# Kernel tuning notes

Hardware: AMD Instinct MI355X
Metric: run time of the kernel (lower is better)

The kernel has to match this reference:

```python
import jax, jax.numpy as jnp
import numpy as np


def setup_inputs() -> dict:
    key = jax.random.key(0)
    ks = jax.random.split(key, 8)
    C, dk = 256, 32
    B, H, W = 4, 64, 64
    x = jax.random.normal(ks[0], (B, C, H, W), dtype=jnp.float32)
    wq = jax.random.normal(ks[1], (dk, C), dtype=jnp.float32) * (1.0 / np.sqrt(C))
    bq = jnp.zeros((dk,), dtype=jnp.float32)
    wk = jax.random.normal(ks[2], (dk, C), dtype=jnp.float32) * (1.0 / np.sqrt(C))
    bk = jnp.zeros((dk,), dtype=jnp.float32)
    wv = jax.random.normal(ks[3], (C, C), dtype=jnp.float32) * (1.0 / np.sqrt(C))
    bv = jnp.zeros((C,), dtype=jnp.float32)
    gamma = jnp.ones((1,), dtype=jnp.float32)
    return {"x": x, "wq": wq, "bq": bq, "wk": wk, "bk": bk,
            "wv": wv, "bv": bv, "gamma": gamma}


def reference(x, wq, bq, wk, bk, wv, bv, gamma):
    B, C, H, W = x.shape
    N = H * W
    xf = x.reshape(B, C, N)  # [B, C, N]
    # 1x1 convs == per-pixel linear projections
    q = jnp.einsum('dc,bcn->bnd', wq, xf) + bq  # [B, N, dk]  (proj_query, permuted)
    k = jnp.einsum('dc,bcn->bdn', wk, xf) + bk[None, :, None]  # [B, dk, N]
    v = jnp.einsum('ec,bcn->ben', wv, xf) + bv[None, :, None]  # [B, C, N]
    energy = jnp.einsum('bnd,bdm->bnm', q, k)  # [B, N, N]
    attention = jax.nn.softmax(energy, axis=-1)
    # out[b,c,i] = sum_j v[b,c,j] * attention[b,i,j]
    out = jnp.einsum('bcj,bij->bci', v, attention)  # [B, C, N]
    out = out.reshape(B, C, H, W)
    return gamma[0] * out + x
```

## Files before the change

### kernel.cpp

```cpp
#include <hip/hip_runtime.h>

#define NPIX 4096
#define CIN  256
#define DK   32

typedef __attribute__((ext_vector_type(8))) short short8;
typedef __attribute__((ext_vector_type(16))) float f32x16;

__device__ __forceinline__ unsigned short f2bf(float f) {
    unsigned int u = __float_as_uint(f);
    return (unsigned short)((u + 0x7fffu + ((u >> 16) & 1u)) >> 16);
}
__device__ __forceinline__ float bf2f(unsigned short h) {
    return __uint_as_float(((unsigned int)h) << 16);
}

__global__ void wprep_kernel(const float* __restrict__ wq, const float* __restrict__ wk,
                             const float* __restrict__ wv,
                             unsigned short* __restrict__ wqh, unsigned short* __restrict__ wql,
                             unsigned short* __restrict__ wkh, unsigned short* __restrict__ wkl,
                             unsigned short* __restrict__ wvh) {
    const int lane = threadIdx.x & 63, li = lane & 31, hi = lane >> 5;
    const int kc = blockIdx.x, y = blockIdx.y;
    if (y < 4) {
        const float* m = (y < 2) ? wq : wk;
        short8 h8, l8;
#pragma unroll
        for (int e = 0; e < 8; ++e) {
            float v = m[li * CIN + kc * 16 + hi * 8 + e];
            unsigned short hb = f2bf(v);
            h8[e] = (short)hb;
            l8[e] = (short)f2bf(v - bf2f(hb));
        }
        unsigned short* dst = (y == 0) ? wqh : (y == 1) ? wql : (y == 2) ? wkh : wkl;
        *reinterpret_cast<short8*>(&dst[kc * 512 + lane * 8]) = (y & 1) ? l8 : h8;
    } else {
        const int cblk = y - 4;
        short8 h8;
#pragma unroll
        for (int e = 0; e < 8; ++e)
            h8[e] = (short)f2bf(wv[(cblk * 32 + li) * CIN + kc * 16 + hi * 8 + e]);
        *reinterpret_cast<short8*>(&wvh[(cblk * 16 + kc) * 512 + lane * 8]) = h8;
    }
}

__global__ __launch_bounds__(512) void projall_kernel(
        const float* __restrict__ x,
        const unsigned short* __restrict__ wqh, const unsigned short* __restrict__ wql,
        const unsigned short* __restrict__ wkh, const unsigned short* __restrict__ wkl,
        const unsigned short* __restrict__ wvh,
        const float* __restrict__ bq, const float* __restrict__ bk, const float* __restrict__ bv,
        unsigned short* __restrict__ qfrag, unsigned short* __restrict__ kfrag,
        unsigned short* __restrict__ vfrag) {
    __shared__ float xs[64][36];
    __shared__ unsigned short xhf[16 * 512];
    __shared__ unsigned short xlf[16 * 512];
    __shared__ unsigned short ts[2][32][40];

    const int t = threadIdx.x, lane = t & 63, li = lane & 31, hi = lane >> 5, w = t >> 6;
    const int nblk = blockIdx.x, b = blockIdx.y;
    const int n0 = nblk * 32;

    for (int cb = 0; cb < 4; ++cb) {
        {
            int c = t >> 3, n4 = (t & 7) * 4;
            float4 v = *reinterpret_cast<const float4*>(
                &x[(size_t)(b * CIN + cb * 64 + c) * NPIX + n0 + n4]);
            xs[c][n4 + 0] = v.x; xs[c][n4 + 1] = v.y;
            xs[c][n4 + 2] = v.z; xs[c][n4 + 3] = v.w;
        }
        __syncthreads();
        {
            const int kc = w & 3;
            const bool isL = (w >= 4);
            short8 f;
#pragma unroll
            for (int e = 0; e < 8; ++e) {
                float v = xs[kc * 16 + hi * 8 + e][li];
                unsigned short hb = f2bf(v);
                f[e] = isL ? (short)f2bf(v - bf2f(hb)) : (short)hb;
            }
            unsigned short* dst = isL ? xlf : xhf;
            *reinterpret_cast<short8*>(&dst[(cb * 4 + kc) * 512 + lane * 8]) = f;
        }
        __syncthreads();
    }

    if (w < 2) {
        const unsigned short* wh = (w == 0) ? wqh : wkh;
        const unsigned short* wl = (w == 0) ? wql : wkl;
        const float* bias = (w == 0) ? bq : bk;
        f32x16 acc;
#pragma unroll
        for (int r = 0; r < 16; ++r) acc[r] = 0.f;
        for (int kc = 0; kc < 16; ++kc) {
            short8 ah = *reinterpret_cast<const short8*>(&xhf[kc * 512 + lane * 8]);
            short8 al = *reinterpret_cast<const short8*>(&xlf[kc * 512 + lane * 8]);
            short8 whf = *reinterpret_cast<const short8*>(&wh[kc * 512 + lane * 8]);
            short8 wlf = *reinterpret_cast<const short8*>(&wl[kc * 512 + lane * 8]);
            acc = __builtin_amdgcn_mfma_f32_32x32x16_bf16(ah, whf, acc, 0, 0, 0);
            acc = __builtin_amdgcn_mfma_f32_32x32x16_bf16(al, whf, acc, 0, 0, 0);
            acc = __builtin_amdgcn_mfma_f32_32x32x16_bf16(ah, wlf, acc, 0, 0, 0);
        }
        const float bs = bias[li];
#pragma unroll
        for (int r = 0; r < 16; ++r) {
            int row = (r & 3) + 8 * (r >> 2) + 4 * hi;
            ts[w][row][li] = f2bf(acc[r] + bs);
        }
        unsigned short* dstf = (w == 0) ? qfrag : kfrag;
#pragma unroll
        for (int dh = 0; dh < 2; ++dh) {
            short8 f = *reinterpret_cast<const short8*>(&ts[w][li][dh * 16 + hi * 8]);
            *reinterpret_cast<short8*>(
                &dstf[((size_t)(b * 128 + nblk) * 2 + dh) * 512 + lane * 8]) = f;
        }
    } else {
        const int w2 = w - 2;
        const int njob = (w2 < 2) ? 2 : 1;
        for (int jj = 0; jj < njob; ++jj) {
            const int cblk = w2 + jj * 6;
            f32x16 acc;
#pragma unroll
            for (int r = 0; r < 16; ++r) acc[r] = 0.f;
            for (int kc = 0; kc < 16; ++kc) {
                short8 xb = *reinterpret_cast<const short8*>(&xhf[kc * 512 + lane * 8]);
                short8 wf = *reinterpret_cast<const short8*>(&wvh[(cblk * 16 + kc) * 512 + lane * 8]);
                acc = __builtin_amdgcn_mfma_f32_32x32x16_bf16(xb, wf, acc, 0, 0, 0);
            }
            const float bvv = bv[cblk * 32 + li];
#pragma unroll
            for (int g = 0; g < 2; ++g) {
                short8 sv;
#pragma unroll
                for (int e = 0; e < 8; ++e) sv[e] = (short)f2bf(acc[g * 8 + e] + bvv);
                *reinterpret_cast<short8*>(
                    &vfrag[((size_t)(b * 8 + cblk) * 256 + nblk * 2 + g) * 512 + lane * 8]) = sv;
            }
        }
    }
}

__global__ __launch_bounds__(768, 6) void attnv_kernel(
        const unsigned short* __restrict__ qfrag, const unsigned short* __restrict__ kfrag,
        const unsigned short* __restrict__ vfrag, unsigned short* __restrict__ opart,
        float* __restrict__ lpart, float* __restrict__ out) {
    __shared__ unsigned short Ps[4 * 8 * 512];
    __shared__ float sred[2][4][32];

    const int t = threadIdx.x, lane = t & 63, li = lane & 31, hi = lane >> 5, w = t >> 6;
    const int blk = blockIdx.x;
    const int xcd = blk & 7, slot = blk >> 3;
    const int jh = slot & 1, ps = slot >> 1;
    const int b = xcd >> 1;
    const int ipos = (xcd & 1) * 32 + ps;

    if (w < 4) {
        const int sl = w & 3;
        short8 qb[2][2];
#pragma unroll
        for (int it = 0; it < 2; ++it) {
            size_t qoff = ((size_t)(b * 128 + ipos * 2 + it) * 2) * 512 + lane * 8;
            qb[it][0] = *reinterpret_cast<const short8*>(&qfrag[qoff]);
            qb[it][1] = *reinterpret_cast<const short8*>(&qfrag[qoff + 512]);
        }
        float ssum[2] = {0.f, 0.f};

        auto do_E = [&](int s) {
            const int buf = s & 1;
            size_t koff = ((size_t)(b * 128 + jh * 64 + s * 4 + sl) * 2) * 512 + lane * 8;
            short8 k0 = *reinterpret_cast<const short8*>(&kfrag[koff]);
            short8 k1 = *reinterpret_cast<const short8*>(&kfrag[koff + 512]);
#pragma unroll
            for (int it = 0; it < 2; ++it) {
                f32x16 e;
#pragma unroll
                for (int r = 0; r < 16; ++r) e[r] = 0.f;
                e = __builtin_amdgcn_mfma_f32_32x32x16_bf16(k0, qb[it][0], e, 0, 0, 0);
                e = __builtin_amdgcn_mfma_f32_32x32x16_bf16(k1, qb[it][1], e, 0, 0, 0);
#pragma unroll
                for (int g = 0; g < 2; ++g) {
                    short8 pv8;
#pragma unroll
                    for (int e2 = 0; e2 < 8; ++e2) {
                        float pe = __expf(e[g * 8 + e2]);
                        ssum[it] += pe;
                        pv8[e2] = (short)f2bf(pe);
                    }
                    *reinterpret_cast<short8*>(
                        &Ps[((it * 2 + buf) * 8 + sl * 2 + g) * 512 + lane * 8]) = pv8;
                }
            }
        };

        do_E(0);
        __syncthreads();
#pragma unroll 1
        for (int s = 0; s < 16; ++s) {
            if (s + 1 < 16) do_E(s + 1);
            __syncthreads();
        }
#pragma unroll
        for (int it = 0; it < 2; ++it) {
            ssum[it] += __shfl_xor(ssum[it], 32);
            if (lane < 32) sred[it][sl][li] = ssum[it];
        }
        __syncthreads();
        if (sl == 0 && lane < 32) {
#pragma unroll
            for (int it = 0; it < 2; ++it) {
                float lt = sred[it][0][li] + sred[it][1][li] + sred[it][2][li] + sred[it][3][li];
                lpart[((size_t)jh * 4 + b) * NPIX + ipos * 64 + it * 32 + li] = lt;
            }
        }
    } else {
        const int cq = w - 4;
        f32x16 acc0, acc1;
#pragma unroll
        for (int r = 0; r < 16; ++r) { acc0[r] = 0.f; acc1[r] = 0.f; }

        __syncthreads();
#pragma unroll 1
        for (int s = 0; s < 16; ++s) {
            const int buf = s & 1;
            size_t vbase = ((size_t)(b * 8 + cq) * 256 + jh * 128 + s * 8) * 512 + lane * 8;
            short8 vcur = *reinterpret_cast<const short8*>(&vfrag[vbase]);
#pragma unroll
            for (int kc = 0; kc < 8; ++kc) {
                short8 vnext;
                if (kc < 7) vnext = *reinterpret_cast<const short8*>(&vfrag[vbase + (kc + 1) * 512]);
                short8 B0 = *reinterpret_cast<const short8*>(&Ps[(buf * 8 + kc) * 512 + lane * 8]);
                short8 B1 = *reinterpret_cast<const short8*>(&Ps[((2 + buf) * 8 + kc) * 512 + lane * 8]);
                acc0 = __builtin_amdgcn_mfma_f32_32x32x16_bf16(vcur, B0, acc0, 0, 0, 0);
                acc1 = __builtin_amdgcn_mfma_f32_32x32x16_bf16(vcur, B1, acc1, 0, 0, 0);
                vcur = vnext;
            }
            __syncthreads();
        }
        __syncthreads();

#pragma unroll
        for (int it = 0; it < 2; ++it) {
            const f32x16& A = it ? acc1 : acc0;
#pragma unroll
            for (int r = 0; r < 16; ++r) {
                int c = cq * 32 + (r & 3) + 8 * (r >> 2) + 4 * hi;
                size_t idx = (size_t)(b * CIN + c) * NPIX + ipos * 64 + it * 32 + li;
                if (jh == 0) out[idx] = A[r];
                else         opart[idx] = f2bf(A[r]);
            }
        }
    }
}

__global__ __launch_bounds__(256) void merge_kernel(
        const unsigned short* __restrict__ opart, const float* __restrict__ lpart,
        const float* __restrict__ xin, const float* __restrict__ gamma,
        float* __restrict__ out) {
    const size_t idx4 = ((size_t)blockIdx.x * 256 + threadIdx.x) * 4;
    const size_t i  = idx4 & (NPIX - 1);
    const size_t b  = idx4 >> 20;
    float4 o0 = *reinterpret_cast<const float4*>(&out[idx4]);
    float4 xv = *reinterpret_cast<const float4*>(&xin[idx4]);
    float4 l0 = *reinterpret_cast<const float4*>(&lpart[b * NPIX + i]);
    float4 l1 = *reinterpret_cast<const float4*>(&lpart[(4 + b) * NPIX + i]);
    const unsigned short* op = &opart[idx4];
    const float g = gamma[0];
    float4 o;
    o.x = g * (o0.x + bf2f(op[0])) / (l0.x + l1.x) + xv.x;
    o.y = g * (o0.y + bf2f(op[1])) / (l0.y + l1.y) + xv.y;
    o.z = g * (o0.z + bf2f(op[2])) / (l0.z + l1.z) + xv.z;
    o.w = g * (o0.w + bf2f(op[3])) / (l0.w + l1.w) + xv.w;
    *reinterpret_cast<float4*>(&out[idx4]) = o;
}

extern "C" void kernel_launch(void* const* d_in, const int* in_sizes, int n_in,
                              void* d_out, int out_size, void* d_ws, size_t ws_size,
                              hipStream_t stream) {
    const float* x     = (const float*)d_in[0];
    const float* wq    = (const float*)d_in[1];
    const float* bq    = (const float*)d_in[2];
    const float* wk    = (const float*)d_in[3];
    const float* bk    = (const float*)d_in[4];
    const float* wv    = (const float*)d_in[5];
    const float* bv    = (const float*)d_in[6];
    const float* gamma = (const float*)d_in[7];
    float* out = (float*)d_out;

    unsigned short* qf    = (unsigned short*)d_ws;
    unsigned short* kf    = qf + (size_t)524288;
    unsigned short* vf    = kf + (size_t)524288;
    unsigned short* wqh   = vf + (size_t)4194304;
    unsigned short* wql   = wqh + 8192;
    unsigned short* wkh   = wql + 8192;
    unsigned short* wkl   = wkh + 8192;
    unsigned short* wvh   = wkl + 8192;
    unsigned short* opart = wvh + 65536;
    float*          lpart = (float*)(opart + 4194304);

    wprep_kernel<<<dim3(16, 12), 64, 0, stream>>>(wq, wk, wv, wqh, wql, wkh, wkl, wvh);
    projall_kernel<<<dim3(128, 4), 512, 0, stream>>>(x, wqh, wql, wkh, wkl, wvh,
                                                     bq, bk, bv, qf, kf, vf);
    attnv_kernel<<<dim3(512), 768, 0, stream>>>(qf, kf, vf, opart, lpart, out);
    merge_kernel<<<dim3(4096), 256, 0, stream>>>(opart, lpart, x, gamma, out);
}
```

Before: 145.4 us.

## Give each PV wave two channel blocks and shrink attention block to 512 threads

The attention kernel drops from 8 consumer waves (one 32-channel block each) to 4 consumer waves that each own two channel blocks. Each P fragment read from LDS now feeds four MFMAs instead of two, halving LDS traffic per MFMA, and the block becomes 512 threads with adjusted launch bounds. The exp/bf16 packing also switches to a paired float2-to-bf16x2 intrinsic with a tree sum. The cost is more accumulator registers per wave, and the explicit software prefetch of V fragments is gone, so global load latency may be less hidden.

Measured after the change: 143.6 us. Within noise of the previous version (-1.2%).

```diff
diff --git a/kernel.cpp b/kernel.cpp
--- a/kernel.cpp
+++ b/kernel.cpp
@@ -1,4 +1,5 @@
 #include <hip/hip_runtime.h>
+#include <hip/hip_bf16.h>
 
 #define NPIX 4096
 #define CIN  256
@@ -13,6 +14,12 @@
 }
 __device__ __forceinline__ float bf2f(unsigned short h) {
     return __uint_as_float(((unsigned int)h) << 16);
+}
+__device__ __forceinline__ unsigned int f2bf2(float a, float b) {
+    __hip_bfloat162 h = __float22bfloat162_rn(make_float2(a, b));
+    unsigned int u;
+    __builtin_memcpy(&u, &h, 4);
+    return u;
 }
 
 __global__ void wprep_kernel(const float* __restrict__ wq, const float* __restrict__ wk,
@@ -141,7 +148,7 @@
     }
 }
 
-__global__ __launch_bounds__(768, 6) void attnv_kernel(
+__global__ __launch_bounds__(512, 4) void attnv_kernel(
         const unsigned short* __restrict__ qfrag, const unsigned short* __restrict__ kfrag,
         const unsigned short* __restrict__ vfrag, unsigned short* __restrict__ opart,
         float* __restrict__ lpart, float* __restrict__ out) {
@@ -156,7 +163,7 @@
     const int ipos = (xcd & 1) * 32 + ps;
 
     if (w < 4) {
-        const int sl = w & 3;
+        const int sl = w;
         short8 qb[2][2];
 #pragma unroll
         for (int it = 0; it < 2; ++it) {
@@ -180,15 +187,16 @@
                 e = __builtin_amdgcn_mfma_f32_32x32x16_bf16(k1, qb[it][1], e, 0, 0, 0);
 #pragma unroll
                 for (int g = 0; g < 2; ++g) {
-                    short8 pv8;
-#pragma unroll
-                    for (int e2 = 0; e2 < 8; ++e2) {
-                        float pe = __expf(e[g * 8 + e2]);
-                        ssum[it] += pe;
-                        pv8[e2] = (short)f2bf(pe);
-                    }
-                    *reinterpret_cast<short8*>(
-                        &Ps[((it * 2 + buf) * 8 + sl * 2 + g) * 512 + lane * 8]) = pv8;
+                    float p0 = __expf(e[g * 8 + 0]), p1 = __expf(e[g * 8 + 1]);
+                    float p2 = __expf(e[g * 8 + 2]), p3 = __expf(e[g * 8 + 3]);
+                    float p4 = __expf(e[g * 8 + 4]), p5 = __expf(e[g * 8 + 5]);
+                    float p6 = __expf(e[g * 8 + 6]), p7 = __expf(e[g * 8 + 7]);
+                    ssum[it] += ((p0 + p1) + (p2 + p3)) + ((p4 + p5) + (p6 + p7));
+                    uint4 pk;
+                    pk.x = f2bf2(p0, p1); pk.y = f2bf2(p2, p3);
+                    pk.z = f2bf2(p4, p5); pk.w = f2bf2(p6, p7);
+                    *reinterpret_cast<uint4*>(
+                        &Ps[((it * 2 + buf) * 8 + sl * 2 + g) * 512 + lane * 8]) = pk;
                 }
             }
         };
@@ -214,40 +222,47 @@
             }
         }
     } else {
-        const int cq = w - 4;
-        f32x16 acc0, acc1;
-#pragma unroll
-        for (int r = 0; r < 16; ++r) { acc0[r] = 0.f; acc1[r] = 0.f; }
+        const int cq2 = w - 4;
+        f32x16 acc00, acc01, acc10, acc11;
+#pragma unroll
+        for (int r = 0; r < 16; ++r) { acc00[r] = 0.f; acc01[r] = 0.f; acc10[r] = 0.f; acc11[r] = 0.f; }
 
         __syncthreads();
 #pragma unroll 1
         for (int s = 0; s < 16; ++s) {
             const int buf = s & 1;
-            size_t vbase = ((size_t)(b * 8 + cq) * 256 + jh * 128 + s * 8) * 512 + lane * 8;
-            short8 vcur = *reinterpret_cast<const short8*>(&vfrag[vbase]);
+            size_t vb0 = ((size_t)(b * 8 + cq2 * 2)     * 256 + jh * 128 + s * 8) * 512 + lane * 8;
+            size_t vb1 = ((size_t)(b * 8 + cq2 * 2 + 1) * 256 + jh * 128 + s * 8) * 512 + lane * 8;
+            const unsigned short* p0 = &Ps[(buf * 8) * 512 + lane * 8];
+            const unsigned short* p1 = &Ps[((2 + buf) * 8) * 512 + lane * 8];
 #pragma unroll
             for (int kc = 0; kc < 8; ++kc) {
-                short8 vnext;
-                if (kc < 7) vnext = *reinterpret_cast<const short8*>(&vfrag[vbase + (kc + 1) * 512]);
-                short8 B0 = *reinterpret_cast<const short8*>(&Ps[(buf * 8 + kc) * 512 + lane * 8]);
-                short8 B1 = *reinterpret_cast<const short8*>(&Ps[((2 + buf) * 8 + kc) * 512 + lane * 8]);
-                acc0 = __builtin_amdgcn_mfma_f32_32x32x16_bf16(vcur, B0, acc0, 0, 0, 0);
-                acc1 = __builtin_amdgcn_mfma_f32_32x32x16_bf16(vcur, B1, acc1, 0, 0, 0);
-                vcur = vnext;
+                short8 B0 = *reinterpret_cast<const short8*>(p0 + kc * 512);
+                short8 B1 = *reinterpret_cast<const short8*>(p1 + kc * 512);
+                short8 v0 = *reinterpret_cast<const short8*>(&vfrag[vb0 + kc * 512]);
+                short8 v1 = *reinterpret_cast<const short8*>(&vfrag[vb1 + kc * 512]);
+                acc00 = __builtin_amdgcn_mfma_f32_32x32x16_bf16(v0, B0, acc00, 0, 0, 0);
+                acc01 = __builtin_amdgcn_mfma_f32_32x32x16_bf16(v0, B1, acc01, 0, 0, 0);
+                acc10 = __builtin_amdgcn_mfma_f32_32x32x16_bf16(v1, B0, acc10, 0, 0, 0);
+                acc11 = __builtin_amdgcn_mfma_f32_32x32x16_bf16(v1, B1, acc11, 0, 0, 0);
             }
             __syncthreads();
         }
         __syncthreads();
 
 #pragma unroll
-        for (int it = 0; it < 2; ++it) {
-            const f32x16& A = it ? acc1 : acc0;
-#pragma unroll
-            for (int r = 0; r < 16; ++r) {
-                int c = cq * 32 + (r & 3) + 8 * (r >> 2) + 4 * hi;
-                size_t idx = (size_t)(b * CIN + c) * NPIX + ipos * 64 + it * 32 + li;
-                if (jh == 0) out[idx] = A[r];
-                else         opart[idx] = f2bf(A[r]);
+        for (int cs = 0; cs < 2; ++cs) {
+#pragma unroll
+            for (int it = 0; it < 2; ++it) {
+                const f32x16& A = (cs == 0) ? (it == 0 ? acc00 : acc01)
+                                            : (it == 0 ? acc10 : acc11);
+#pragma unroll
+                for (int r = 0; r < 16; ++r) {
+                    int c = cq2 * 64 + cs * 32 + (r & 3) + 8 * (r >> 2) + 4 * hi;
+                    size_t idx = (size_t)(b * CIN + c) * NPIX + ipos * 64 + it * 32 + li;
+                    if (jh == 0) out[idx] = A[r];
+                    else         opart[idx] = f2bf(A[r]);
+                }
             }
         }
     }
@@ -301,6 +316,6 @@
     wprep_kernel<<<dim3(16, 12), 64, 0, stream>>>(wq, wk, wv, wqh, wql, wkh, wkl, wvh);
     projall_kernel<<<dim3(128, 4), 512, 0, stream>>>(x, wqh, wql, wkh, wkl, wvh,
                                                      bq, bk, bv, qf, kf, vf);
-    attnv_kernel<<<dim3(512), 768, 0, stream>>>(qf, kf, vf, opart, lpart, out);
+    attnv_kernel<<<dim3(512), 512, 0, stream>>>(qf, kf, vf, opart, lpart, out);
     merge_kernel<<<dim3(4096), 256, 0, stream>>>(opart, lpart, x, gamma, out);
 }
```
